# Performance work log

Hardware: AMD Instinct MI355X
Metric: run time of the kernel (lower is better)

Reference implementation:

```python
import jax, jax.numpy as jnp
import numpy as np

NUM_EMBEDDINGS = 1024
EMBEDDING_DIM = 256
COMMITMENT_COST = 0.25
DECAY = 0.99
EPSILON = 1e-5


def setup_inputs() -> dict:
    key = jax.random.key(0)
    k1, k2 = jax.random.split(key)
    B, C, D, H, W = 4, EMBEDDING_DIM, 16, 32, 32
    z = jax.random.normal(k1, (B, C, D, H, W), dtype=jnp.float32)
    bound = 1.0 / (EMBEDDING_DIM ** 0.5)  # nn.init.uniform_(-1/sqrt(d), 1/sqrt(d))
    embed = jax.random.uniform(k2, (NUM_EMBEDDINGS, EMBEDDING_DIM), dtype=jnp.float32,
                               minval=-bound, maxval=bound)
    ema_cluster_size = jnp.zeros((NUM_EMBEDDINGS,), dtype=jnp.float32)
    ema_embed_sum = embed  # buffer initialized as a clone of the embedding weight
    return {"z": z, "embed": embed,
            "ema_cluster_size": ema_cluster_size, "ema_embed_sum": ema_embed_sum}


def reference(z, embed, ema_cluster_size, ema_embed_sum):
    """Training-mode forward of VectorQuantizer (EMA codebook update included).

    Returns (z_q [B,C,D,H,W], vq_loss scalar, indices [B,D,H,W]).
    """
    K, Dm = embed.shape
    B, C, D, H, W = z.shape
    # (B,C,D,H,W) -> (B,D,H,W,C) -> (N, Dm)
    zp = jnp.transpose(z, (0, 2, 3, 4, 1))
    zf = zp.reshape(-1, Dm)

    # squared-distance via expanded cdist: |z|^2 + |e|^2 - 2 z e^T
    dist = (jnp.sum(zf * zf, axis=1, keepdims=True)
            + jnp.sum(embed * embed, axis=1)
            - 2.0 * jnp.matmul(zf, embed.T))  # (N, K)
    idx = jnp.argmin(dist, axis=1)  # (N,)

    # EMA statistics (one-hot matmuls expressed as segment sums)
    batch_cluster_size = jax.ops.segment_sum(jnp.ones_like(idx, dtype=zf.dtype), idx,
                                             num_segments=K)
    batch_embed_sum = jax.ops.segment_sum(zf, idx, num_segments=K)  # (K, Dm)
    new_ema_cs = DECAY * ema_cluster_size + (1.0 - DECAY) * batch_cluster_size
    new_ema_es = DECAY * ema_embed_sum + (1.0 - DECAY) * batch_embed_sum
    n = jnp.sum(new_ema_cs)
    cluster_size = (new_ema_cs + EPSILON) / (n + K * EPSILON) * n
    new_embed = new_ema_es / cluster_size[:, None]  # updated codebook, used for gather

    z_q = new_embed[idx].reshape(zp.shape)  # (B,D,H,W,C)
    vq_loss = COMMITMENT_COST * jnp.mean((zp - jax.lax.stop_gradient(z_q)) ** 2)
    z_q = zp + jax.lax.stop_gradient(z_q - zp)  # straight-through

    indices = idx.reshape(B, D, H, W)
    z_q = jnp.transpose(z_q, (0, 4, 1, 2, 3))  # back to (B,C,D,H,W)
    return z_q, vq_loss, indices
```

## Files before the change

### kernel.cpp

```cpp
#include <hip/hip_runtime.h>
#include <hip/hip_bf16.h>
#include <cfloat>

#define NTOT    65536
#define KCODES  1024
#define DM      256
#define SPAT    16384
#define ZQ_SIZE 16777216

#define WS_ENORM 0
#define WS_CSIZE 1024
#define WS_START 2048
#define WS_LOSSP 3104
#define WS_HIST  11296
#define WS_SORT  273440
#define WS_IDX   338976
#define WS_NEWE  404512

#define GLOAD_LDS16(gp, lp) __builtin_amdgcn_global_load_lds( \
    (const __attribute__((address_space(1))) unsigned int*)(gp), \
    (__attribute__((address_space(3))) unsigned int*)(lp), 16, 0, 0)

__global__ __launch_bounds__(256) void enorm_kernel(const float* __restrict__ embed,
                                                    float* __restrict__ enorm) {
    int k = blockIdx.x;
    int t = threadIdx.x;
    float v = embed[k * DM + t];
    v *= v;
    #pragma unroll
    for (int m = 32; m > 0; m >>= 1) v += __shfl_xor(v, m);
    __shared__ float sm[4];
    if ((t & 63) == 0) sm[t >> 6] = v;
    __syncthreads();
    if (t == 0) enorm[k] = sm[0] + sm[1] + sm[2] + sm[3];
}

__global__ __launch_bounds__(256, 4) void argmin_kernel(
    const float* __restrict__ z, const float* __restrict__ embed,
    const float* __restrict__ enorm, int* __restrict__ idx_out,
    float* __restrict__ dout, float* __restrict__ zt) {
    __shared__ __align__(16) float zs[2][16][64];
    __shared__ __align__(16) float es[2][128][16];

    const int tid = threadIdx.x;
    const int n0  = blockIdx.x * 64;
    const int b   = n0 >> 14;
    const int s0  = n0 & 16383;
    const int ti  = tid >> 4;
    const int tj  = tid & 15;
    const int w   = tid >> 6;
    const int l   = tid & 63;

    auto stage_z = [&](int st, int buf) {
        const int c0 = (st & 15) * 16;
        int cc = c0 + w * 4 + (l >> 4);
        const float* gp = z + (size_t)(b * DM + cc) * SPAT + s0 + (l & 15) * 4;
        GLOAD_LDS16(gp, &zs[buf][w * 4][0]);
    };
    auto stage_es = [&](int st, int buf) {
        const int k0 = (st >> 4) * 128;
        const int c0 = (st & 15) * 16;
        #pragma unroll
        for (int v = 0; v < 2; ++v) {
            int R = w * 32 + v * 16;
            int sg = (l & 3) ^ ((l >> 3) & 3);
            const float* gp = embed + (size_t)(k0 + R + (l >> 2)) * DM + c0 + sg * 4;
            GLOAD_LDS16(gp, &es[buf][R][0]);
        }
    };

    stage_z(0, 0);
    stage_es(0, 0);

    float best[4], acc[4][8];
    int   bestk[4];
    #pragma unroll
    for (int i = 0; i < 4; ++i) { best[i] = FLT_MAX; bestk[i] = 0; }

    #pragma unroll 1
    for (int st = 0; st < 128; ++st) {
        const int buf = st & 1;
        const int k0  = (st >> 4) * 128;

        __syncthreads();

        if (st < 127) { stage_z(st + 1, buf ^ 1); stage_es(st + 1, buf ^ 1); }

        if (st < 16) {
            const int c0 = st * 16;
            int r = tid >> 2, cg = tid & 3;
            float4 v4;
            v4.x = zs[buf][cg * 4 + 0][r];
            v4.y = zs[buf][cg * 4 + 1][r];
            v4.z = zs[buf][cg * 4 + 2][r];
            v4.w = zs[buf][cg * 4 + 3][r];
            *(float4*)&zt[(size_t)(n0 + r) * DM + c0 + cg * 4] = v4;
        }

        if ((st & 15) == 0) {
            #pragma unroll
            for (int i = 0; i < 4; ++i)
                #pragma unroll
                for (int j = 0; j < 8; ++j) acc[i][j] = 0.f;
        }

        #pragma unroll
        for (int cq = 0; cq < 4; ++cq) {
            float4 zq[4];
            #pragma unroll
            for (int q = 0; q < 4; ++q)
                zq[q] = *(const float4*)&zs[buf][cq * 4 + q][ti * 4];
            const int eoff = ((cq ^ ((tj >> 1) & 3)) << 2);
            #pragma unroll
            for (int j = 0; j < 8; ++j) {
                float4 eb = *(const float4*)&es[buf][tj + j * 16][eoff];
                #pragma unroll
                for (int q = 0; q < 4; ++q) {
                    float ec = (q == 0) ? eb.x : (q == 1) ? eb.y
                             : (q == 2) ? eb.z : eb.w;
                    acc[0][j] = fmaf(zq[q].x, ec, acc[0][j]);
                    acc[1][j] = fmaf(zq[q].y, ec, acc[1][j]);
                    acc[2][j] = fmaf(zq[q].z, ec, acc[2][j]);
                    acc[3][j] = fmaf(zq[q].w, ec, acc[3][j]);
                }
            }
        }

        if ((st & 15) == 15) {
            #pragma unroll
            for (int j = 0; j < 8; ++j) {
                int q = k0 + tj + j * 16;
                float en = enorm[q];
                #pragma unroll
                for (int i = 0; i < 4; ++i) {
                    float v = fmaf(-2.0f, acc[i][j], en);
                    if (v < best[i]) { best[i] = v; bestk[i] = q; }
                }
            }
        }
    }

    #pragma unroll
    for (int i = 0; i < 4; ++i) {
        float bd = best[i];
        int   bk = bestk[i];
        #pragma unroll
        for (int m = 1; m < 16; m <<= 1) {
            float od = __shfl_xor(bd, m);
            int   ok = __shfl_xor(bk, m);
            if (od < bd || (od == bd && ok < bk)) { bd = od; bk = ok; }
        }
        if (tj == 0) {
            int n = n0 + ti * 4 + i;
            idx_out[n] = bk;
            dout[ZQ_SIZE + 1 + n] = (float)bk;
        }
    }
}

__global__ __launch_bounds__(256) void hist_kernel(const int* __restrict__ idx,
                                                   int* __restrict__ hist) {
    __shared__ int lh[KCODES];
    int ch = blockIdx.x, t = threadIdx.x;
    #pragma unroll
    for (int u = 0; u < 4; ++u) lh[t + u * 256] = 0;
    __syncthreads();
    int k = idx[ch * 256 + t];
    atomicAdd(&lh[k], 1);
    __syncthreads();
    #pragma unroll
    for (int u = 0; u < 4; ++u)
        hist[ch * KCODES + t + u * 256] = lh[t + u * 256];
}

__global__ __launch_bounds__(1024) void scan_kernel(
    int* __restrict__ hist, const float* __restrict__ ema_cs,
    int* __restrict__ start, float* __restrict__ csize) {
    int k = threadIdx.x;
    int run = 0;
    for (int ch = 0; ch < 256; ++ch) {
        int t = hist[ch * KCODES + k];
        hist[ch * KCODES + k] = run;
        run += t;
    }
    int lane = k & 63, wv = k >> 6;
    int v = run;
    #pragma unroll
    for (int d = 1; d < 64; d <<= 1) {
        int t = __shfl_up(v, d);
        if (lane >= d) v += t;
    }
    __shared__ int wsum[16];
    if (lane == 63) wsum[wv] = v;
    __syncthreads();
    __shared__ int wpre[16];
    if (k == 0) {
        int s = 0;
        #pragma unroll
        for (int i = 0; i < 16; ++i) { wpre[i] = s; s += wsum[i]; }
    }
    __syncthreads();
    int excl = wpre[wv] + v - run;
    start[k] = excl;
    if (k == 1023) start[1024] = excl + run;
    float ncs = 0.99f * ema_cs[k] + 0.01f * (float)run;
    float r = ncs;
    #pragma unroll
    for (int m = 32; m > 0; m >>= 1) r += __shfl_xor(r, m);
    __shared__ float fs[16];
    if (lane == 0) fs[wv] = r;
    __syncthreads();
    __shared__ float nt;
    if (k == 0) {
        float s = 0.f;
        #pragma unroll
        for (int i = 0; i < 16; ++i) s += fs[i];
        nt = s;
    }
    __syncthreads();
    float n = nt;
    csize[k] = (ncs + 1e-5f) / (n + 1024.0f * 1e-5f) * n;
}

__global__ __launch_bounds__(256) void rank_scatter_kernel(
    const int* __restrict__ idx, const int* __restrict__ hist,
    const int* __restrict__ start, int* __restrict__ sorted) {
    __shared__ int lidx[256];
    int ch = blockIdx.x, t = threadIdx.x;
    int k = idx[ch * 256 + t];
    lidx[t] = k;
    __syncthreads();
    int rank = 0;
    for (int j = 0; j < 255; ++j)
        if (j < t && lidx[j] == k) ++rank;
    sorted[start[k] + hist[ch * KCODES + k] + rank] = ch * 256 + t;
}

__global__ __launch_bounds__(256) void gather_kernel(
    const float* __restrict__ zt, const int* __restrict__ sorted,
    const int* __restrict__ start, const float* __restrict__ ema_es,
    const float* __restrict__ csize, float* __restrict__ newe) {
    int k = blockIdx.x, c = threadIdx.x;
    int s0 = start[k], s1 = start[k + 1];
    float acc = 0.f;
    for (int i = s0; i < s1; ++i) {
        int n = sorted[i];
        acc += zt[(size_t)n * DM + c];
    }
    size_t o = (size_t)k * DM + c;
    newe[o] = (0.99f * ema_es[o] + 0.01f * acc) / csize[k];
}

__global__ __launch_bounds__(256) void output_kernel(
    const float* __restrict__ z, const float* __restrict__ newe,
    const int* __restrict__ idx, float* __restrict__ dout,
    float* __restrict__ lossp) {
    int gid = blockIdx.x * 256 + threadIdx.x;
    float lsum = 0.f;
    #pragma unroll
    for (int it = 0; it < 8; ++it) {
        int o = gid + it * (8192 * 256);
        int s = o & 16383, t2 = o >> 14;
        int c = t2 & 255, b = t2 >> 8;
        int n = (b << 14) + s;
        int k = idx[n];
        float v = newe[(size_t)k * DM + c];
        float zv = z[o];
        dout[o] = v;
        float d = zv - v;
        lsum = fmaf(d, d, lsum);
    }
    #pragma unroll
    for (int m = 32; m > 0; m >>= 1) lsum += __shfl_xor(lsum, m);
    __shared__ float sm[4];
    int t = threadIdx.x;
    if ((t & 63) == 0) sm[t >> 6] = lsum;
    __syncthreads();
    if (t == 0) lossp[blockIdx.x] = sm[0] + sm[1] + sm[2] + sm[3];
}

__global__ __launch_bounds__(256) void loss_final_kernel(const float* __restrict__ lossp,
                                                         float* __restrict__ dout) {
    int t = threadIdx.x;
    float v = 0.f;
    for (int i = t; i < 8192; i += 256) v += lossp[i];
    #pragma unroll
    for (int m = 32; m > 0; m >>= 1) v += __shfl_xor(v, m);
    __shared__ float sm[4];
    if ((t & 63) == 0) sm[t >> 6] = v;
    __syncthreads();
    if (t == 0) dout[ZQ_SIZE] = 0.25f * ((sm[0] + sm[1] + sm[2] + sm[3]) / 16777216.0f);
}

extern "C" void kernel_launch(void* const* d_in, const int* in_sizes, int n_in,
                              void* d_out, int out_size, void* d_ws, size_t ws_size,
                              hipStream_t stream) {
    const float* z      = (const float*)d_in[0];
    const float* embed  = (const float*)d_in[1];
    const float* ema_cs = (const float*)d_in[2];
    const float* ema_es = (const float*)d_in[3];
    float* out = (float*)d_out;
    float* ws  = (float*)d_ws;

    float* enorm = ws + WS_ENORM;
    float* csize = ws + WS_CSIZE;
    int*   start = (int*)(ws + WS_START);
    float* lossp = ws + WS_LOSSP;
    int*   hist  = (int*)(ws + WS_HIST);
    int*   sortd = (int*)(ws + WS_SORT);
    int*   idx   = (int*)(ws + WS_IDX);
    float* newe  = ws + WS_NEWE;
    float* zt    = out;

    enorm_kernel<<<KCODES, 256, 0, stream>>>(embed, enorm);
    argmin_kernel<<<NTOT / 64, 256, 0, stream>>>(z, embed, enorm, idx, out, zt);
    hist_kernel<<<256, 256, 0, stream>>>(idx, hist);
    scan_kernel<<<1, 1024, 0, stream>>>(hist, ema_cs, start, csize);
    rank_scatter_kernel<<<256, 256, 0, stream>>>(idx, hist, start, sortd);
    gather_kernel<<<KCODES, 256, 0, stream>>>(zt, sortd, start, ema_es, csize, newe);
    output_kernel<<<8192, 256, 0, stream>>>(z, newe, idx, out, lossp);
    loss_final_kernel<<<1, 256, 0, stream>>>(lossp, out);
}
```

Before: 643.3 us.

## Triple-buffer argmin LDS staging with explicit vmcnt waits and raised compute priority

The argmin kernel's shared-memory staging moves from double to triple buffering, prefetching two stages ahead. The full __syncthreads is replaced by an explicit s_waitcnt vmcnt(3) plus s_barrier, so one stage's loads can stay in flight. The FMA loop is wrapped in s_setprio to favour compute waves. This adds LDS use (about 36KB per block at 4 blocks/CU), and the vmcnt count depends on the exact number of global loads issued per stage.

```diff
diff --git a/kernel.cpp b/kernel.cpp
--- a/kernel.cpp
+++ b/kernel.cpp
@@ -39,8 +39,8 @@
     const float* __restrict__ z, const float* __restrict__ embed,
     const float* __restrict__ enorm, int* __restrict__ idx_out,
     float* __restrict__ dout, float* __restrict__ zt) {
-    __shared__ __align__(16) float zs[2][16][64];
-    __shared__ __align__(16) float es[2][128][16];
+    __shared__ __align__(16) float zs[3][16][64];
+    __shared__ __align__(16) float es[3][128][16];
 
     const int tid = threadIdx.x;
     const int n0  = blockIdx.x * 64;
@@ -71,29 +71,41 @@
 
     stage_z(0, 0);
     stage_es(0, 0);
+    stage_z(1, 1);
+    stage_es(1, 1);
 
     float best[4], acc[4][8];
     int   bestk[4];
     #pragma unroll
     for (int i = 0; i < 4; ++i) { best[i] = FLT_MAX; bestk[i] = 0; }
 
+    int cur = 0;
     #pragma unroll 1
     for (int st = 0; st < 128; ++st) {
-        const int buf = st & 1;
-        const int k0  = (st >> 4) * 128;
-
-        __syncthreads();
-
-        if (st < 127) { stage_z(st + 1, buf ^ 1); stage_es(st + 1, buf ^ 1); }
+        const int k0 = (st >> 4) * 128;
+
+        if (st == 127) {
+            asm volatile("s_waitcnt vmcnt(0)" ::: "memory");
+        } else {
+            asm volatile("s_waitcnt vmcnt(3)" ::: "memory");
+        }
+        __builtin_amdgcn_s_barrier();
+        __builtin_amdgcn_sched_barrier(0);
+
+        if (st + 2 < 128) {
+            int nb = (cur >= 1) ? cur - 1 : cur + 2;
+            stage_z(st + 2, nb);
+            stage_es(st + 2, nb);
+        }
 
         if (st < 16) {
             const int c0 = st * 16;
             int r = tid >> 2, cg = tid & 3;
             float4 v4;
-            v4.x = zs[buf][cg * 4 + 0][r];
-            v4.y = zs[buf][cg * 4 + 1][r];
-            v4.z = zs[buf][cg * 4 + 2][r];
-            v4.w = zs[buf][cg * 4 + 3][r];
+            v4.x = zs[cur][cg * 4 + 0][r];
+            v4.y = zs[cur][cg * 4 + 1][r];
+            v4.z = zs[cur][cg * 4 + 2][r];
+            v4.w = zs[cur][cg * 4 + 3][r];
             *(float4*)&zt[(size_t)(n0 + r) * DM + c0 + cg * 4] = v4;
         }
 
@@ -104,16 +116,17 @@
                 for (int j = 0; j < 8; ++j) acc[i][j] = 0.f;
         }
 
+        __builtin_amdgcn_s_setprio(1);
         #pragma unroll
         for (int cq = 0; cq < 4; ++cq) {
             float4 zq[4];
             #pragma unroll
             for (int q = 0; q < 4; ++q)
-                zq[q] = *(const float4*)&zs[buf][cq * 4 + q][ti * 4];
+                zq[q] = *(const float4*)&zs[cur][cq * 4 + q][ti * 4];
             const int eoff = ((cq ^ ((tj >> 1) & 3)) << 2);
             #pragma unroll
             for (int j = 0; j < 8; ++j) {
-                float4 eb = *(const float4*)&es[buf][tj + j * 16][eoff];
+                float4 eb = *(const float4*)&es[cur][tj + j * 16][eoff];
                 #pragma unroll
                 for (int q = 0; q < 4; ++q) {
                     float ec = (q == 0) ? eb.x : (q == 1) ? eb.y
@@ -125,6 +138,7 @@
                 }
             }
         }
+        __builtin_amdgcn_s_setprio(0);
 
         if ((st & 15) == 15) {
             #pragma unroll
@@ -138,6 +152,8 @@
                 }
             }
         }
+
+        cur = (cur == 2) ? 0 : cur + 1;
     }
 
     #pragma unroll
```

Result: slower. 684.9 us (+6.5%).

## Split argmin codebook search across two blocks and merge partial minima

Applied to the files above, without the earlier changes.

The argmin kernel now launches twice as many blocks, each scanning half of the codebook for a 64-row tile, and writes per-half best distance and index to workspace. A new merge kernel then picks the smaller of the two and writes the final index. This is meant to raise parallelism and occupancy: the launch-bounds hint goes from 4 to 6 waves and s_setprio is raised around the FMA loop. In exchange the z tile is loaded twice, a small extra kernel launch is added, and the two halves are merged with a strict less-than, so ties resolve to the lower half as before.

```diff
diff --git a/kernel.cpp b/kernel.cpp
--- a/kernel.cpp
+++ b/kernel.cpp
@@ -16,6 +16,8 @@
 #define WS_SORT  273440
 #define WS_IDX   338976
 #define WS_NEWE  404512
+#define WS_BDIST 666656
+#define WS_BIDX  797728
 
 #define GLOAD_LDS16(gp, lp) __builtin_amdgcn_global_load_lds( \
     (const __attribute__((address_space(1))) unsigned int*)(gp), \
@@ -35,15 +37,17 @@
     if (t == 0) enorm[k] = sm[0] + sm[1] + sm[2] + sm[3];
 }
 
-__global__ __launch_bounds__(256, 4) void argmin_kernel(
+__global__ __launch_bounds__(256, 6) void argmin_kernel(
     const float* __restrict__ z, const float* __restrict__ embed,
-    const float* __restrict__ enorm, int* __restrict__ idx_out,
-    float* __restrict__ dout, float* __restrict__ zt) {
+    const float* __restrict__ enorm, float* __restrict__ bdist,
+    int* __restrict__ bidx, float* __restrict__ zt) {
     __shared__ __align__(16) float zs[2][16][64];
     __shared__ __align__(16) float es[2][128][16];
 
     const int tid = threadIdx.x;
-    const int n0  = blockIdx.x * 64;
+    const int bx  = blockIdx.x;
+    const int kh  = bx & 1;
+    const int n0  = (bx >> 1) * 64;
     const int b   = n0 >> 14;
     const int s0  = n0 & 16383;
     const int ti  = tid >> 4;
@@ -58,7 +62,7 @@
         GLOAD_LDS16(gp, &zs[buf][w * 4][0]);
     };
     auto stage_es = [&](int st, int buf) {
-        const int k0 = (st >> 4) * 128;
+        const int k0 = kh * 512 + (st >> 4) * 128;
         const int c0 = (st & 15) * 16;
         #pragma unroll
         for (int v = 0; v < 2; ++v) {
@@ -78,15 +82,15 @@
     for (int i = 0; i < 4; ++i) { best[i] = FLT_MAX; bestk[i] = 0; }
 
     #pragma unroll 1
-    for (int st = 0; st < 128; ++st) {
+    for (int st = 0; st < 64; ++st) {
         const int buf = st & 1;
-        const int k0  = (st >> 4) * 128;
+        const int k0  = kh * 512 + (st >> 4) * 128;
 
         __syncthreads();
 
-        if (st < 127) { stage_z(st + 1, buf ^ 1); stage_es(st + 1, buf ^ 1); }
-
-        if (st < 16) {
+        if (st < 63) { stage_z(st + 1, buf ^ 1); stage_es(st + 1, buf ^ 1); }
+
+        if (kh == 0 && st < 16) {
             const int c0 = st * 16;
             int r = tid >> 2, cg = tid & 3;
             float4 v4;
@@ -104,6 +108,7 @@
                 for (int j = 0; j < 8; ++j) acc[i][j] = 0.f;
         }
 
+        __builtin_amdgcn_s_setprio(1);
         #pragma unroll
         for (int cq = 0; cq < 4; ++cq) {
             float4 zq[4];
@@ -125,6 +130,7 @@
                 }
             }
         }
+        __builtin_amdgcn_s_setprio(0);
 
         if ((st & 15) == 15) {
             #pragma unroll
@@ -152,10 +158,20 @@
         }
         if (tj == 0) {
             int n = n0 + ti * 4 + i;
-            idx_out[n] = bk;
-            dout[ZQ_SIZE + 1 + n] = (float)bk;
-        }
-    }
+            bdist[kh * NTOT + n] = bd;
+            bidx[kh * NTOT + n]  = bk;
+        }
+    }
+}
+
+__global__ __launch_bounds__(256) void merge_kernel(
+    const float* __restrict__ bdist, const int* __restrict__ bidx,
+    int* __restrict__ idx, float* __restrict__ dout) {
+    int n = blockIdx.x * 256 + threadIdx.x;
+    float d0 = bdist[n], d1 = bdist[NTOT + n];
+    int k = (d1 < d0) ? bidx[NTOT + n] : bidx[n];
+    idx[n] = k;
+    dout[ZQ_SIZE + 1 + n] = (float)k;
 }
 
 __global__ __launch_bounds__(256) void hist_kernel(const int* __restrict__ idx,
@@ -310,10 +326,13 @@
     int*   sortd = (int*)(ws + WS_SORT);
     int*   idx   = (int*)(ws + WS_IDX);
     float* newe  = ws + WS_NEWE;
+    float* bdist = ws + WS_BDIST;
+    int*   bidx  = (int*)(ws + WS_BIDX);
     float* zt    = out;
 
     enorm_kernel<<<KCODES, 256, 0, stream>>>(embed, enorm);
-    argmin_kernel<<<NTOT / 64, 256, 0, stream>>>(z, embed, enorm, idx, out, zt);
+    argmin_kernel<<<NTOT / 64 * 2, 256, 0, stream>>>(z, embed, enorm, bdist, bidx, zt);
+    merge_kernel<<<NTOT / 256, 256, 0, stream>>>(bdist, bidx, idx, out);
     hist_kernel<<<256, 256, 0, stream>>>(idx, hist);
     scan_kernel<<<1, 1024, 0, stream>>>(hist, ema_cs, start, csize);
     rank_scatter_kernel<<<256, 256, 0, stream>>>(idx, hist, start, sortd);
```

Result: slower. 826.5 us (+28.5%).
